# Performance work log

Hardware: AMD Instinct MI355X
Metric: run time of the kernel (lower is better)

Reference implementation:

```python
import math
import jax, jax.numpy as jnp
import numpy as np

B, R, C = 128, 196, 2048   # batch, regions, encoder channels
H, A = 1024, 1024          # decoder hidden, attention dim


def setup_inputs() -> dict:
    key = jax.random.key(0)
    ks = jax.random.split(key, 6)
    s_e = 1.0 / math.sqrt(C)
    s_d = 1.0 / math.sqrt(H)
    s_f = 1.0 / math.sqrt(2 * A)
    return {
        "image": jax.random.normal(ks[0], (B, R, C), dtype=jnp.float32),
        "decoder_hidden": jax.random.normal(ks[1], (B, H), dtype=jnp.float32),
        "We": jax.random.normal(ks[2], (A, C), dtype=jnp.float32) * s_e,
        "be": jnp.zeros((A,), dtype=jnp.float32),
        "Wd": jax.random.normal(ks[3], (A, H), dtype=jnp.float32) * s_d,
        "bd": jnp.zeros((A,), dtype=jnp.float32),
        "Wf": jax.random.normal(ks[4], (1, 2 * A), dtype=jnp.float32) * s_f,
        "bf": jnp.zeros((1,), dtype=jnp.float32),
    }


def gelu_exact(x):
    # x * 0.5 * (1 + erf(x / sqrt(2))) — matches the torch erf-based gelu
    return jax.nn.gelu(x, approximate=False)


def reference(image, decoder_hidden, We, be, Wd, bd, Wf, bf):
    # encoder_att: [B, R, C] @ We^T -> [B, R, A]
    attn_1 = jnp.einsum("brc,ac->bra", image, We) + be
    # decoder_att: [B, H] @ Wd^T -> [B, A], broadcast over regions
    attn_2 = decoder_hidden @ Wd.T + bd               # [B, A]
    # full_att on concat([attn_1, attn_2]) == split the [1, 2A] weight
    Wf1, Wf2 = Wf[:, :A], Wf[:, A:]                   # each [1, A]
    g1 = gelu_exact(attn_1)                           # [B, R, A]
    g2 = gelu_exact(attn_2)                           # [B, A]
    scores = jnp.einsum("bra,a->br", g1, Wf1[0]) + (g2 @ Wf2[0])[:, None] + bf[0]
    alpha = jax.nn.softmax(scores, axis=1)            # softmax over regions
    attended_image = jnp.einsum("brc,br->bc", image, alpha)  # [B, C]
    return attended_image, alpha
```

## Files before the change

### kernel.cpp

```cpp
#include <hip/hip_runtime.h>
#include <math.h>

#define B_ 128
#define R_ 196
#define C_ 2048
#define A_ 1024
#define M_ (B_*R_)
#define NIMG ((size_t)M_*C_)
#define NTOT (NIMG + (size_t)A_*C_)

typedef short short8 __attribute__((ext_vector_type(8)));
typedef float f32x4  __attribute__((ext_vector_type(4)));

#define AS1 __attribute__((address_space(1)))
#define AS3 __attribute__((address_space(3)))

__device__ __forceinline__ short f2bf(float f) {
    unsigned u = __builtin_bit_cast(unsigned, f);
    u = (u + 0x7fffu + ((u >> 16) & 1u)) >> 16;
    return (short)u;
}

__device__ __forceinline__ short8 pack8(const float4 a, const float4 b) {
    short8 r;
    r[0]=f2bf(a.x); r[1]=f2bf(a.y); r[2]=f2bf(a.z); r[3]=f2bf(a.w);
    r[4]=f2bf(b.x); r[5]=f2bf(b.y); r[6]=f2bf(b.z); r[7]=f2bf(b.w);
    return r;
}

__device__ __forceinline__ float gelu_exact(float x) {
    return 0.5f * x * (1.0f + erff(x * 0.70710678118654752f));
}

__global__ __launch_bounds__(256) void tobf16_k(const float* __restrict__ img,
                                                const float* __restrict__ We,
                                                ushort* __restrict__ dst)
{
    size_t i = ((size_t)blockIdx.x * blockDim.x + threadIdx.x) * 8;
    const size_t stride = (size_t)gridDim.x * blockDim.x * 8;
    for (; i < NTOT; i += stride) {
        const float* s = (i < NIMG) ? (img + i) : (We + (i - NIMG));
        const float4 a = ((const float4*)s)[0];
        const float4 b = ((const float4*)s)[1];
        *(short8*)(dst + i) = pack8(a, b);
    }
}

__global__ __launch_bounds__(256, 3) void score_gemm_bf16(
    const ushort* __restrict__ Abf, const ushort* __restrict__ Bbf,
    const float* __restrict__ be,   const float* __restrict__ Wf,
    float* __restrict__ scores)
{
    __shared__ ushort ldsA[128*64];
    __shared__ ushort ldsB[128*64];

    const int t    = threadIdx.x;
    const int lane = t & 63;
    const int wid  = t >> 6;

    const int L     = ((blockIdx.x & 7) * 196) + (blockIdx.x >> 3);
    const int mtile = L >> 3;
    const int ntile = L & 7;
    const int m0 = mtile * 128;
    const int n0 = ntile * 128;

    int soff[4];
    #pragma unroll
    for (int i = 0; i < 4; i++) {
        const int sidx = (wid*4 + i)*64 + lane;
        const int row  = sidx >> 3;
        const int kk   = (sidx & 7) ^ (row & 7);
        soff[i] = row*4096 + kk*16;
    }
    const char* Ap = (const char*)Abf + (size_t)m0 * 4096;
    const char* Bp = (const char*)Bbf + (size_t)n0 * 4096;
    char* lA = (char*)ldsA;
    char* lB = (char*)ldsB;
    const int lbase = wid * 4096;

    const int wr = wid >> 1, wc = wid & 1;
    const int r16 = lane & 15, kg = lane >> 4;

    int arow[4], brow[4];
    #pragma unroll
    for (int mi = 0; mi < 4; mi++) arow[mi] = wr*64 + mi*16 + r16;
    #pragma unroll
    for (int ni = 0; ni < 4; ni++) brow[ni] = wc*64 + ni*16 + r16;

    f32x4 acc[4][4];
    #pragma unroll
    for (int i = 0; i < 4; i++)
        #pragma unroll
        for (int j = 0; j < 4; j++) acc[i][j] = f32x4{0.f,0.f,0.f,0.f};

    const short8* sA = (const short8*)ldsA;
    const short8* sB = (const short8*)ldsB;

    for (int kt = 0; kt < 32; ++kt) {
        __syncthreads();
        const int kb = kt * 128;
        #pragma unroll
        for (int i = 0; i < 4; i++)
            __builtin_amdgcn_global_load_lds((AS1 void*)(Ap + soff[i] + kb),
                                             (AS3 void*)(lA + lbase + i*1024), 16, 0, 0);
        #pragma unroll
        for (int i = 0; i < 4; i++)
            __builtin_amdgcn_global_load_lds((AS1 void*)(Bp + soff[i] + kb),
                                             (AS3 void*)(lB + lbase + i*1024), 16, 0, 0);
        __syncthreads();

        #pragma unroll
        for (int s = 0; s < 2; s++) {
            short8 af[4], bfr[4];
            const int kk = s*4 + kg;
            #pragma unroll
            for (int mi = 0; mi < 4; mi++)
                af[mi] = sA[arow[mi]*8 + (kk ^ (arow[mi] & 7))];
            #pragma unroll
            for (int ni = 0; ni < 4; ni++)
                bfr[ni] = sB[brow[ni]*8 + (kk ^ (brow[ni] & 7))];
            #pragma unroll
            for (int mi = 0; mi < 4; mi++)
                #pragma unroll
                for (int ni = 0; ni < 4; ni++)
                    acc[mi][ni] = __builtin_amdgcn_mfma_f32_16x16x32_bf16(af[mi], bfr[ni], acc[mi][ni], 0, 0, 0);
        }
    }

    float rowsum[4][4];
    #pragma unroll
    for (int mi = 0; mi < 4; mi++)
        #pragma unroll
        for (int i = 0; i < 4; i++) rowsum[mi][i] = 0.f;

    const int colbase = n0 + wc*64 + r16;
    #pragma unroll
    for (int ni = 0; ni < 4; ni++) {
        const int n_g = colbase + ni*16;
        const float ben = be[n_g];
        const float wfn = Wf[n_g];
        #pragma unroll
        for (int mi = 0; mi < 4; mi++)
            #pragma unroll
            for (int i = 0; i < 4; i++)
                rowsum[mi][i] += gelu_exact(acc[mi][ni][i] + ben) * wfn;
    }

    #pragma unroll
    for (int mi = 0; mi < 4; mi++)
        #pragma unroll
        for (int i = 0; i < 4; i++) {
            float v = rowsum[mi][i];
            v += __shfl_xor(v, 1);
            v += __shfl_xor(v, 2);
            v += __shfl_xor(v, 4);
            v += __shfl_xor(v, 8);
            if (r16 == 0) {
                const int row_g = m0 + wr*64 + mi*16 + kg*4 + i;
                atomicAdd(&scores[row_g], v);
            }
        }
}

__global__ __launch_bounds__(256, 2) void score_gemm(
    const float* __restrict__ image, const float* __restrict__ We,
    const float* __restrict__ be,    const float* __restrict__ Wf,
    float* __restrict__ scores)
{
    __shared__ short8 ldsA[1024];
    __shared__ short8 ldsB[1024];

    const int t     = threadIdx.x;
    const int mtile = blockIdx.x >> 3;
    const int ntile = blockIdx.x & 7;
    const int m0 = mtile * 128;
    const int n0 = ntile * 128;

    const int srow = t >> 1;
    const int skh  = t & 1;
    const float* pA = image + (size_t)(m0 + srow) * C_ + skh * 32;
    const float* pB = We    + (size_t)(n0 + srow) * C_ + skh * 32;
    const int wbase = srow * 8 + skh * 4;
    const int wswz  = srow & 7;

    const int lane = t & 63;
    const int wid  = t >> 6;
    const int wr = wid >> 1, wc = wid & 1;
    const int r16 = lane & 15, kg = lane >> 4;

    f32x4 acc[4][4];
    #pragma unroll
    for (int i = 0; i < 4; i++)
        #pragma unroll
        for (int j = 0; j < 4; j++) acc[i][j] = f32x4{0.f,0.f,0.f,0.f};

    float4 ga[8], gb[8];
    #pragma unroll
    for (int j = 0; j < 8; j++) { ga[j] = ((const float4*)pA)[j]; gb[j] = ((const float4*)pB)[j]; }
    pA += 64; pB += 64;

    for (int kt = 0; kt < 32; ++kt) {
        #pragma unroll
        for (int s = 0; s < 4; s++) {
            ldsA[(wbase + s) ^ wswz] = pack8(ga[2*s], ga[2*s+1]);
            ldsB[(wbase + s) ^ wswz] = pack8(gb[2*s], gb[2*s+1]);
        }
        __syncthreads();
        if (kt < 31) {
            #pragma unroll
            for (int j = 0; j < 8; j++) { ga[j] = ((const float4*)pA)[j]; gb[j] = ((const float4*)pB)[j]; }
            pA += 64; pB += 64;
        }
        short8 af[4][2], bfr[4][2];
        #pragma unroll
        for (int mi = 0; mi < 4; mi++) {
            const int row = wr*64 + mi*16 + r16;
            const int base = row*8 + kg;
            const int sw = row & 7;
            af[mi][0] = ldsA[ base      ^ sw];
            af[mi][1] = ldsA[(base + 4) ^ sw];
        }
        #pragma unroll
        for (int ni = 0; ni < 4; ni++) {
            const int row = wc*64 + ni*16 + r16;
            const int base = row*8 + kg;
            const int sw = row & 7;
            bfr[ni][0] = ldsB[ base      ^ sw];
            bfr[ni][1] = ldsB[(base + 4) ^ sw];
        }
        #pragma unroll
        for (int mi = 0; mi < 4; mi++)
            #pragma unroll
            for (int ni = 0; ni < 4; ni++) {
                acc[mi][ni] = __builtin_amdgcn_mfma_f32_16x16x32_bf16(af[mi][0], bfr[ni][0], acc[mi][ni], 0, 0, 0);
                acc[mi][ni] = __builtin_amdgcn_mfma_f32_16x16x32_bf16(af[mi][1], bfr[ni][1], acc[mi][ni], 0, 0, 0);
            }
        __syncthreads();
    }

    float rowsum[4][4];
    #pragma unroll
    for (int mi = 0; mi < 4; mi++)
        #pragma unroll
        for (int i = 0; i < 4; i++) rowsum[mi][i] = 0.f;

    const int colbase = n0 + wc*64 + r16;
    #pragma unroll
    for (int ni = 0; ni < 4; ni++) {
        const int n_g = colbase + ni*16;
        const float ben = be[n_g];
        const float wfn = Wf[n_g];
        #pragma unroll
        for (int mi = 0; mi < 4; mi++)
            #pragma unroll
            for (int i = 0; i < 4; i++)
                rowsum[mi][i] += gelu_exact(acc[mi][ni][i] + ben) * wfn;
    }

    #pragma unroll
    for (int mi = 0; mi < 4; mi++)
        #pragma unroll
        for (int i = 0; i < 4; i++) {
            float v = rowsum[mi][i];
            v += __shfl_xor(v, 1);
            v += __shfl_xor(v, 2);
            v += __shfl_xor(v, 4);
            v += __shfl_xor(v, 8);
            if (r16 == 0) {
                const int row_g = m0 + wr*64 + mi*16 + kg*4 + i;
                atomicAdd(&scores[row_g], v);
            }
        }
}

__global__ void softmax_k(float* __restrict__ scores)
{
    const int b = blockIdx.x;
    const int t = threadIdx.x;
    float v = (t < R_) ? scores[b * R_ + t] : -3.4e38f;

    float m = v;
    #pragma unroll
    for (int off = 1; off < 64; off <<= 1) m = fmaxf(m, __shfl_xor(m, off));
    __shared__ float redm[4];
    if ((t & 63) == 0) redm[t >> 6] = m;
    __syncthreads();
    m = fmaxf(fmaxf(redm[0], redm[1]), fmaxf(redm[2], redm[3]));

    float e = (t < R_) ? expf(v - m) : 0.f;
    float s = e;
    #pragma unroll
    for (int off = 1; off < 64; off <<= 1) s += __shfl_xor(s, off);
    __shared__ float reds[4];
    if ((t & 63) == 0) reds[t >> 6] = s;
    __syncthreads();
    s = reds[0] + reds[1] + reds[2] + reds[3];

    if (t < R_) scores[b * R_ + t] = e / s;
}

__global__ void attend_k(const float* __restrict__ image,
                         const float* __restrict__ alpha,
                         float* __restrict__ out)
{
    const int b     = blockIdx.y;
    const int chunk = blockIdx.x;
    const int t     = threadIdx.x;

    __shared__ float sal[R_];
    if (t < R_) sal[t] = alpha[b * R_ + t];
    __syncthreads();

    const int c = chunk * 1024 + t * 4;
    const float* base = image + (size_t)b * R_ * C_ + c;
    float4 accv = {0.f, 0.f, 0.f, 0.f};
    #pragma unroll 4
    for (int r = 0; r < R_; ++r) {
        const float4 v = *(const float4*)(base + (size_t)r * C_);
        const float a = sal[r];
        accv.x += a * v.x;
        accv.y += a * v.y;
        accv.z += a * v.z;
        accv.w += a * v.w;
    }
    *(float4*)(out + b * C_ + c) = accv;
}

extern "C" void kernel_launch(void* const* d_in, const int* in_sizes, int n_in,
                              void* d_out, int out_size, void* d_ws, size_t ws_size,
                              hipStream_t stream) {
    const float* image = (const float*)d_in[0];
    const float* We    = (const float*)d_in[2];
    const float* be    = (const float*)d_in[3];
    const float* Wf    = (const float*)d_in[6];

    float* out   = (float*)d_out;
    float* alpha = out + (size_t)B_ * C_;

    hipMemsetAsync(alpha, 0, (size_t)M_ * sizeof(float), stream);

    if (ws_size >= NTOT * 2) {
        ushort* Abf = (ushort*)d_ws;
        ushort* Bbf = Abf + NIMG;
        tobf16_k<<<dim3(2048), dim3(256), 0, stream>>>(image, We, Abf);
        score_gemm_bf16<<<dim3(196*8), dim3(256), 0, stream>>>(Abf, Bbf, be, Wf, alpha);
    } else {
        score_gemm<<<dim3(196*8), dim3(256), 0, stream>>>(image, We, be, Wf, alpha);
    }
    softmax_k<<<dim3(B_), dim3(256), 0, stream>>>(alpha);
    attend_k<<<dim3(2, B_), dim3(256), 0, stream>>>(image, alpha, out);
}
```

Before: 512.4 us.

## Double-buffer GEMM LDS staging, flatten bf16 conversion grid, retile attend kernel

The score GEMM now uses two LDS buffers, so the global-to-LDS load of the next K tile is issued before the MFMAs on the current tile, with one wait and barrier per iteration instead of two syncthreads. This is meant to hide global load latency, at the cost of doubling LDS to 64KB and lowering launch bounds occupancy from 3 to 2 blocks. The bf16 conversion kernel drops its grid-stride loop and launches one thread per 8 elements. The attend kernel is split into 4 chunks of 128 threads per batch to spread the work over more blocks.

```diff
diff --git a/kernel.cpp b/kernel.cpp
--- a/kernel.cpp
+++ b/kernel.cpp
@@ -36,23 +36,19 @@
                                                 const float* __restrict__ We,
                                                 ushort* __restrict__ dst)
 {
-    size_t i = ((size_t)blockIdx.x * blockDim.x + threadIdx.x) * 8;
-    const size_t stride = (size_t)gridDim.x * blockDim.x * 8;
-    for (; i < NTOT; i += stride) {
-        const float* s = (i < NIMG) ? (img + i) : (We + (i - NIMG));
-        const float4 a = ((const float4*)s)[0];
-        const float4 b = ((const float4*)s)[1];
-        *(short8*)(dst + i) = pack8(a, b);
-    }
-}
-
-__global__ __launch_bounds__(256, 3) void score_gemm_bf16(
+    const size_t i = ((size_t)blockIdx.x * 256 + threadIdx.x) * 8;
+    const float* s = (i < NIMG) ? (img + i) : (We + (i - NIMG));
+    const float4 a = ((const float4*)s)[0];
+    const float4 b = ((const float4*)s)[1];
+    *(short8*)(dst + i) = pack8(a, b);
+}
+
+__global__ __launch_bounds__(256, 2) void score_gemm_bf16(
     const ushort* __restrict__ Abf, const ushort* __restrict__ Bbf,
     const float* __restrict__ be,   const float* __restrict__ Wf,
     float* __restrict__ scores)
 {
-    __shared__ ushort ldsA[128*64];
-    __shared__ ushort ldsB[128*64];
+    __shared__ char lds[2][32768];
 
     const int t    = threadIdx.x;
     const int lane = t & 63;
@@ -74,8 +70,6 @@
     }
     const char* Ap = (const char*)Abf + (size_t)m0 * 4096;
     const char* Bp = (const char*)Bbf + (size_t)n0 * 4096;
-    char* lA = (char*)ldsA;
-    char* lB = (char*)ldsB;
     const int lbase = wid * 4096;
 
     const int wr = wid >> 1, wc = wid & 1;
@@ -93,22 +87,31 @@
         #pragma unroll
         for (int j = 0; j < 4; j++) acc[i][j] = f32x4{0.f,0.f,0.f,0.f};
 
-    const short8* sA = (const short8*)ldsA;
-    const short8* sB = (const short8*)ldsB;
+    #define STAGE(BUF, KT) do {                                                  \
+        const int kb_ = (KT) * 128;                                              \
+        char* dA_ = &lds[BUF][0]     + lbase;                                    \
+        char* dB_ = &lds[BUF][16384] + lbase;                                    \
+        _Pragma("unroll")                                                        \
+        for (int i_ = 0; i_ < 4; i_++)                                           \
+            __builtin_amdgcn_global_load_lds((AS1 void*)(Ap + soff[i_] + kb_),   \
+                                             (AS3 void*)(dA_ + i_*1024), 16, 0, 0); \
+        _Pragma("unroll")                                                        \
+        for (int i_ = 0; i_ < 4; i_++)                                           \
+            __builtin_amdgcn_global_load_lds((AS1 void*)(Bp + soff[i_] + kb_),   \
+                                             (AS3 void*)(dB_ + i_*1024), 16, 0, 0); \
+    } while (0)
+
+    STAGE(0, 0);
+    asm volatile("s_waitcnt vmcnt(0)" ::: "memory");
+    __builtin_amdgcn_s_barrier();
+    __builtin_amdgcn_sched_barrier(0);
 
     for (int kt = 0; kt < 32; ++kt) {
-        __syncthreads();
-        const int kb = kt * 128;
-        #pragma unroll
-        for (int i = 0; i < 4; i++)
-            __builtin_amdgcn_global_load_lds((AS1 void*)(Ap + soff[i] + kb),
-                                             (AS3 void*)(lA + lbase + i*1024), 16, 0, 0);
-        #pragma unroll
-        for (int i = 0; i < 4; i++)
-            __builtin_amdgcn_global_load_lds((AS1 void*)(Bp + soff[i] + kb),
-                                             (AS3 void*)(lB + lbase + i*1024), 16, 0, 0);
-        __syncthreads();
-
+        const int cur = kt & 1;
+        if (kt < 31) STAGE(cur ^ 1, kt + 1);
+
+        const short8* sA = (const short8*)&lds[cur][0];
+        const short8* sB = (const short8*)&lds[cur][16384];
         #pragma unroll
         for (int s = 0; s < 2; s++) {
             short8 af[4], bfr[4];
@@ -125,7 +128,14 @@
                 for (int ni = 0; ni < 4; ni++)
                     acc[mi][ni] = __builtin_amdgcn_mfma_f32_16x16x32_bf16(af[mi], bfr[ni], acc[mi][ni], 0, 0, 0);
         }
-    }
+
+        if (kt < 31) {
+            asm volatile("s_waitcnt vmcnt(0)" ::: "memory");
+            __builtin_amdgcn_s_barrier();
+            __builtin_amdgcn_sched_barrier(0);
+        }
+    }
+    #undef STAGE
 
     float rowsum[4][4];
     #pragma unroll
@@ -299,19 +309,22 @@
     if (t < R_) scores[b * R_ + t] = e / s;
 }
 
-__global__ void attend_k(const float* __restrict__ image,
-                         const float* __restrict__ alpha,
-                         float* __restrict__ out)
+__global__ __launch_bounds__(128) void attend_k(const float* __restrict__ image,
+                                                const float* __restrict__ alpha,
+                                                float* __restrict__ out)
 {
     const int b     = blockIdx.y;
     const int chunk = blockIdx.x;
     const int t     = threadIdx.x;
 
     __shared__ float sal[R_];
-    if (t < R_) sal[t] = alpha[b * R_ + t];
+    if (t < R_) {
+        sal[t] = alpha[b * R_ + t];
+        if (t + 128 < R_) sal[t + 128] = alpha[b * R_ + t + 128];
+    }
     __syncthreads();
 
-    const int c = chunk * 1024 + t * 4;
+    const int c = chunk * 512 + t * 4;
     const float* base = image + (size_t)b * R_ * C_ + c;
     float4 accv = {0.f, 0.f, 0.f, 0.f};
     #pragma unroll 4
@@ -342,11 +355,11 @@
     if (ws_size >= NTOT * 2) {
         ushort* Abf = (ushort*)d_ws;
         ushort* Bbf = Abf + NIMG;
-        tobf16_k<<<dim3(2048), dim3(256), 0, stream>>>(image, We, Abf);
+        tobf16_k<<<dim3(26112), dim3(256), 0, stream>>>(image, We, Abf);
         score_gemm_bf16<<<dim3(196*8), dim3(256), 0, stream>>>(Abf, Bbf, be, Wf, alpha);
     } else {
         score_gemm<<<dim3(196*8), dim3(256), 0, stream>>>(image, We, be, Wf, alpha);
     }
     softmax_k<<<dim3(B_), dim3(256), 0, stream>>>(alpha);
-    attend_k<<<dim3(2, B_), dim3(256), 0, stream>>>(image, alpha, out);
-}
+    attend_k<<<dim3(4, B_), dim3(128), 0, stream>>>(image, alpha, out);
+}
```

Measured after the change: 507.4 us. Within noise of the previous version (-1.0%).
